# Kernel optimization log

Measured on AMD Instinct MI355X. Metric: run time of the kernel, lower is better.

The kernel has to match this reference:

```python
import jax, jax.numpy as jnp
import numpy as np

T_DAYS = 1024   # forecast horizon (r_t length)
N_SAMP = 50000  # posterior_samples
J_WIN = 32      # transition_window


def setup_inputs() -> dict:
    key = jax.random.key(0)
    k0, k1, k2, k3, k4, k5 = jax.random.split(key, 6)
    # reproduction number around 1 so the recursion is numerically stable
    r_t = jax.random.uniform(k0, (T_DAYS,), minval=0.9, maxval=1.1, dtype=jnp.float32)
    # J days of warmup asymptomatic counts (one per posterior sample)
    warmup_A = jax.random.uniform(k1, (J_WIN, N_SAMP), minval=10.0, maxval=100.0, dtype=jnp.float32)
    # per-sample epidemiological parameters (reparameterized posterior samples)
    delta = jax.random.uniform(k2, (N_SAMP,), minval=0.95, maxval=1.0, dtype=jnp.float32)
    T_serial = jax.random.uniform(k3, (N_SAMP,), minval=4.0, maxval=7.0, dtype=jnp.float32)
    rho_M = jax.random.uniform(k4, (N_SAMP,), minval=0.05, maxval=0.3, dtype=jnp.float32)
    # lag distribution pi_M[j, s]: normalized over the J lags per sample
    pi_M = jax.nn.softmax(jax.random.normal(k5, (J_WIN, N_SAMP), dtype=jnp.float32), axis=0)
    return {"r_t": r_t, "warmup_A": warmup_A, "delta": delta,
            "T_serial": T_serial, "rho_M": rho_M, "pi_M": pi_M}


def reference(r_t, warmup_A, delta, T_serial, rho_M, pi_M):
    """Covid compartment forecast.

    A[day] = A[day-1] * delta * r_t[day]**(1/T_serial)   (sequential recursion)
    M[day] = sum_j A[day-1-j] * rho_M * pi_M[j]          (lagged transition window)
    Returns M: [T, S] incident mild cases per posterior sample.
    """
    J, S = warmup_A.shape
    T = r_t.shape[0]
    # per-day multiplicative growth factor, [T, S]
    growth = (r_t[:, None] ** (1.0 / T_serial)[None, :]) * delta[None, :]

    def step(a_prev, g):
        a = a_prev * g
        return a, a

    _, A_fc = jax.lax.scan(step, warmup_A[-1], growth)  # [T, S]
    A_full = jnp.concatenate([warmup_A, A_fc], axis=0)  # [J+T, S]

    # M[day] = sum_j A_full[J + day - 1 - j] * rho_M * pi_M[j]
    M = jnp.zeros((T, S), dtype=A_fc.dtype)
    for j in range(J):  # small fixed window, accumulate without [T,J,S] blowup
        start = J - 1 - j
        M = M + A_full[start:start + T] * (rho_M * pi_M[j])[None, :]
    return M
```

## Files before the change

### kernel.cpp

```cpp
#include <hip/hip_runtime.h>
#include <math.h>


#define T_DAYS 1024
#define J_WIN  32
#define DT     128
#define GROUPS (DT / 32)

__global__ void prefix_log_kernel(const float* __restrict__ r_t,
                                  float* __restrict__ L) {
    __shared__ float buf[T_DAYS];
    const int i = threadIdx.x;
    buf[i] = __log2f(r_t[i]);
    __syncthreads();
    for (int off = 1; off < T_DAYS; off <<= 1) {
        float add = (i >= off) ? buf[i - off] : 0.0f;
        __syncthreads();
        buf[i] += add;
        __syncthreads();
    }
    L[i] = buf[i];
}

__global__ __launch_bounds__(256, 4)
void covid_kernel(const float* __restrict__ warmup_A,
                  const float* __restrict__ delta_p,
                  const float* __restrict__ T_serial,
                  const float* __restrict__ rho_p,
                  const float* __restrict__ pi_M,
                  const float* __restrict__ L,
                  float* __restrict__ out,
                  int S) {
    const int s = blockIdx.x * 256 + threadIdx.x;
    if (s >= S) return;
    const int t0 = blockIdx.y * DT;

    const float invT = 1.0f / T_serial[s];
    const float dlt  = delta_p[s];
    const float ld   = __log2f(dlt);
    const float rho  = rho_p[s];
    const float A0   = warmup_A[(J_WIN - 1) * S + s];

    float w[J_WIN];
#pragma unroll
    for (int j = 0; j < J_WIN; ++j) w[j] = rho * pi_M[j * S + s];

    float ring[J_WIN];
    if (t0 == 0) {
#pragma unroll
        for (int k = 0; k < J_WIN; ++k) ring[k] = warmup_A[k * S + s];
    } else {
#pragma unroll
        for (int k = 0; k < J_WIN; ++k) {
            float arg = fmaf(invT, L[t0 - J_WIN + k],
                             (float)(t0 - J_WIN + k + 1) * ld);
            ring[k] = A0 * __builtin_amdgcn_exp2f(arg);
        }
    }

    float c = (float)(t0 + 1) * ld;
    float* op = out + (size_t)t0 * S + s;
    int tg = t0;
#pragma unroll 1
    for (int g = 0; g < GROUPS; ++g) {
#pragma unroll
        for (int u = 0; u < 32; ++u) {
            float m0 = 0.0f, m1 = 0.0f, m2 = 0.0f, m3 = 0.0f;
#pragma unroll
            for (int j = 0; j < J_WIN; j += 4) {
                m0 = fmaf(w[j + 0], ring[(u - 1 - j) & 31], m0);
                m1 = fmaf(w[j + 1], ring[(u - 2 - j) & 31], m1);
                m2 = fmaf(w[j + 2], ring[(u - 3 - j) & 31], m2);
                m3 = fmaf(w[j + 3], ring[(u - 4 - j) & 31], m3);
            }
            op[(size_t)u * S] = (m0 + m1) + (m2 + m3);
            float arg = fmaf(invT, L[tg + u], c);
            ring[u] = A0 * __builtin_amdgcn_exp2f(arg);
            c += ld;
        }
        op += (size_t)32 * S;
        tg += 32;
    }
}

extern "C" void kernel_launch(void* const* d_in, const int* in_sizes, int n_in,
                              void* d_out, int out_size, void* d_ws, size_t ws_size,
                              hipStream_t stream) {
    const float* r_t      = (const float*)d_in[0];
    const float* warmup_A = (const float*)d_in[1];
    const float* delta    = (const float*)d_in[2];
    const float* T_serial = (const float*)d_in[3];
    const float* rho_M    = (const float*)d_in[4];
    const float* pi_M     = (const float*)d_in[5];
    float* out = (float*)d_out;
    float* L   = (float*)d_ws;
    const int S = in_sizes[2];

    prefix_log_kernel<<<1, T_DAYS, 0, stream>>>(r_t, L);

    dim3 grid((S + 255) / 256, T_DAYS / DT);
    covid_kernel<<<grid, 256, 0, stream>>>(warmup_A, delta, T_serial, rho_M,
                                           pi_M, L, out, S);
}
```

Before: 250.7 us.

## Process two samples per thread with packed float2 FMA and smaller time tiles

Each thread now handles two adjacent posterior samples held as float2 vectors, so the convolution FMAs can map to packed FP32 instructions and loads and stores become 8-byte wide. The time tile is halved and blocks shrink to 64 threads, adjusting the grid and launch bounds. This is meant to cut FMA issue count and memory instructions, at the cost of doubled register use for the ring and weights, more redundant ring warmup recomputation per tile, and lower occupancy. Odd S is not handled for the second element.

```diff
diff --git a/kernel.cpp b/kernel.cpp
--- a/kernel.cpp
+++ b/kernel.cpp
@@ -4,8 +4,10 @@
 
 #define T_DAYS 1024
 #define J_WIN  32
-#define DT     128
+#define DT     64
 #define GROUPS (DT / 32)
+
+typedef float f32x2 __attribute__((ext_vector_type(2)));
 
 __global__ void prefix_log_kernel(const float* __restrict__ r_t,
                                   float* __restrict__ L) {
@@ -22,7 +24,7 @@
     L[i] = buf[i];
 }
 
-__global__ __launch_bounds__(256, 4)
+__global__ __launch_bounds__(64, 3)
 void covid_kernel(const float* __restrict__ warmup_A,
                   const float* __restrict__ delta_p,
                   const float* __restrict__ T_serial,
@@ -31,52 +33,69 @@
                   const float* __restrict__ L,
                   float* __restrict__ out,
                   int S) {
-    const int s = blockIdx.x * 256 + threadIdx.x;
+    const int p = blockIdx.x * 64 + threadIdx.x;
+    const int s = 2 * p;
     if (s >= S) return;
     const int t0 = blockIdx.y * DT;
 
-    const float invT = 1.0f / T_serial[s];
-    const float dlt  = delta_p[s];
-    const float ld   = __log2f(dlt);
-    const float rho  = rho_p[s];
-    const float A0   = warmup_A[(J_WIN - 1) * S + s];
+    const f32x2 Ts  = *(const f32x2*)&T_serial[s];
+    const f32x2 dlt = *(const f32x2*)&delta_p[s];
+    const f32x2 rho = *(const f32x2*)&rho_p[s];
+    const f32x2 A0  = *(const f32x2*)&warmup_A[(J_WIN - 1) * S + s];
+    f32x2 invT, ld;
+    invT.x = 1.0f / Ts.x;        invT.y = 1.0f / Ts.y;
+    ld.x   = __log2f(dlt.x);     ld.y   = __log2f(dlt.y);
 
-    float w[J_WIN];
+    f32x2 w[J_WIN];
 #pragma unroll
-    for (int j = 0; j < J_WIN; ++j) w[j] = rho * pi_M[j * S + s];
+    for (int j = 0; j < J_WIN; ++j) {
+        const f32x2 pi2 = *(const f32x2*)&pi_M[j * S + s];
+        w[j].x = rho.x * pi2.x;
+        w[j].y = rho.y * pi2.y;
+    }
 
-    float ring[J_WIN];
+    f32x2 ring[J_WIN];
     if (t0 == 0) {
 #pragma unroll
-        for (int k = 0; k < J_WIN; ++k) ring[k] = warmup_A[k * S + s];
+        for (int k = 0; k < J_WIN; ++k)
+            ring[k] = *(const f32x2*)&warmup_A[k * S + s];
     } else {
 #pragma unroll
         for (int k = 0; k < J_WIN; ++k) {
-            float arg = fmaf(invT, L[t0 - J_WIN + k],
-                             (float)(t0 - J_WIN + k + 1) * ld);
-            ring[k] = A0 * __builtin_amdgcn_exp2f(arg);
+            const float Lk = L[t0 - J_WIN + k];
+            const float dn = (float)(t0 - J_WIN + k + 1);
+            ring[k].x = A0.x * __builtin_amdgcn_exp2f(fmaf(invT.x, Lk, dn * ld.x));
+            ring[k].y = A0.y * __builtin_amdgcn_exp2f(fmaf(invT.y, Lk, dn * ld.y));
         }
     }
 
-    float c = (float)(t0 + 1) * ld;
+    f32x2 c;
+    c.x = (float)(t0 + 1) * ld.x;
+    c.y = (float)(t0 + 1) * ld.y;
     float* op = out + (size_t)t0 * S + s;
     int tg = t0;
 #pragma unroll 1
     for (int g = 0; g < GROUPS; ++g) {
 #pragma unroll
         for (int u = 0; u < 32; ++u) {
-            float m0 = 0.0f, m1 = 0.0f, m2 = 0.0f, m3 = 0.0f;
+            f32x2 m0 = {0.0f, 0.0f}, m1 = {0.0f, 0.0f};
+            f32x2 m2 = {0.0f, 0.0f}, m3 = {0.0f, 0.0f};
 #pragma unroll
             for (int j = 0; j < J_WIN; j += 4) {
-                m0 = fmaf(w[j + 0], ring[(u - 1 - j) & 31], m0);
-                m1 = fmaf(w[j + 1], ring[(u - 2 - j) & 31], m1);
-                m2 = fmaf(w[j + 2], ring[(u - 3 - j) & 31], m2);
-                m3 = fmaf(w[j + 3], ring[(u - 4 - j) & 31], m3);
+                m0 = __builtin_elementwise_fma(w[j + 0], ring[(u - 1 - j) & 31], m0);
+                m1 = __builtin_elementwise_fma(w[j + 1], ring[(u - 2 - j) & 31], m1);
+                m2 = __builtin_elementwise_fma(w[j + 2], ring[(u - 3 - j) & 31], m2);
+                m3 = __builtin_elementwise_fma(w[j + 3], ring[(u - 4 - j) & 31], m3);
             }
-            op[(size_t)u * S] = (m0 + m1) + (m2 + m3);
-            float arg = fmaf(invT, L[tg + u], c);
-            ring[u] = A0 * __builtin_amdgcn_exp2f(arg);
-            c += ld;
+            f32x2 m;
+            m.x = (m0.x + m1.x) + (m2.x + m3.x);
+            m.y = (m0.y + m1.y) + (m2.y + m3.y);
+            *(f32x2*)(op + (size_t)u * S) = m;
+            const float Lu = L[tg + u];
+            ring[u].x = A0.x * __builtin_amdgcn_exp2f(fmaf(invT.x, Lu, c.x));
+            ring[u].y = A0.y * __builtin_amdgcn_exp2f(fmaf(invT.y, Lu, c.y));
+            c.x += ld.x;
+            c.y += ld.y;
         }
         op += (size_t)32 * S;
         tg += 32;
@@ -98,7 +117,8 @@
 
     prefix_log_kernel<<<1, T_DAYS, 0, stream>>>(r_t, L);
 
-    dim3 grid((S + 255) / 256, T_DAYS / DT);
-    covid_kernel<<<grid, 256, 0, stream>>>(warmup_A, delta, T_serial, rho_M,
-                                           pi_M, L, out, S);
+    const int pairs = (S + 1) / 2;
+    dim3 grid((pairs + 63) / 64, T_DAYS / DT);
+    covid_kernel<<<grid, 64, 0, stream>>>(warmup_A, delta, T_serial, rho_M,
+                                          pi_M, L, out, S);
 }
```

New measurement: 431.7 us. +72.2%, slower.
